# Performance work log

Hardware: AMD Instinct MI355X
Metric: run time of the kernel (lower is better)

The kernel has to match this reference:

```python
import jax, jax.numpy as jnp
import numpy as np

DELTA_VAR = 0.5
DELTA_DIST = 1.5
ALPHA, BETA, GAMMA = 1.0, 1.0, 0.001
EPS = 1e-8


def setup_inputs() -> dict:
    key = jax.random.key(0)
    k1, k2 = jax.random.split(key)
    N, D, C = 4_000_000, 16, 64
    features = jax.random.normal(k1, (N, D), dtype=jnp.float32)
    labels = jax.random.randint(k2, (N,), 0, C)  # every cluster id present w.h.p.
    return {"features": features, "labels": labels, "num_clusters": C}


def _discriminative_loss(features, labels, C):
    # per-cluster counts and means (scatter-mean, replaces the boolean-mask loop)
    ones = jnp.ones(features.shape[0], dtype=features.dtype)
    counts = jax.ops.segment_sum(ones, labels, num_segments=C)            # (C,)
    sums = jax.ops.segment_sum(features, labels, num_segments=C)          # (C, D)
    safe_counts = jnp.maximum(counts, 1.0)
    means = sums / safe_counts[:, None]                                   # (C, D)

    # intra-cluster (variance) loss: mean over clusters of mean hinge^2
    dists = jnp.linalg.norm(features - means[labels] + EPS, axis=1)       # (N,)
    hinge2 = jnp.square(jnp.maximum(dists - DELTA_VAR, 0.0))
    per_cluster = jax.ops.segment_sum(hinge2, labels, num_segments=C) / safe_counts
    var_loss = jnp.mean(per_cluster)

    # inter-cluster (distance) loss over all ordered pairs i != j
    diff = means[:, None, :] - means[None, :, :] + EPS                    # (C, C, D)
    pdist = jnp.linalg.norm(diff, axis=-1)                                # (C, C)
    h = jnp.square(jnp.maximum(2.0 * DELTA_DIST - pdist, 0.0))
    h = h * (1.0 - jnp.eye(C, dtype=h.dtype))
    dist_loss = jnp.sum(h) / float(C * (C - 1))

    # regularization: mean centroid norm
    reg_loss = jnp.mean(jnp.linalg.norm(means + EPS, axis=1))

    total = ALPHA * var_loss + BETA * dist_loss + GAMMA * reg_loss
    return jnp.stack([total, var_loss, dist_loss, reg_loss])  # (4,)


def reference(features, labels, num_clusters):
    return _discriminative_loss(features, labels, num_clusters)
```

## Files before the change

kernel.cpp:

```cpp
#include <hip/hip_runtime.h>
#include <math.h>

#define C 64
#define D 16
#define EPSF 1e-8f
#define DVAR 0.5f
#define DDIST 1.5f
#define FPSCALE 65536.0f
#define INV_FPSCALE (1.0f / 65536.0f)
#define VARSCALE 4294967296.0
#define INV_VARSCALE (1.0 / 4294967296.0)

__global__ __launch_bounds__(256) void k_zero(int* ws, int n) {
    int i = blockIdx.x * 256 + threadIdx.x;
    if (i < n) ws[i] = 0;
}

__global__ __launch_bounds__(256) void k_sums(const float4* __restrict__ f4,
                                              const int* __restrict__ labels, int N,
                                              int* __restrict__ g_sums,
                                              unsigned* __restrict__ g_cnt) {
    __shared__ int s_sums[C * 17];
    __shared__ unsigned s_cnt[C];
    int t = threadIdx.x;
    for (int i = t; i < C * 17; i += 256) s_sums[i] = 0;
    if (t < C) s_cnt[t] = 0u;
    __syncthreads();

    int ntiles = (N + 255) >> 8;
    for (int it = blockIdx.x; it < ntiles; it += gridDim.x) {
        int tile = ntiles - 1 - it;
        int p = (tile << 8) + t;
        if (p >= N) continue;
        int c = labels[p] & (C - 1);
        float4 a  = f4[4 * p + 0];
        float4 b  = f4[4 * p + 1];
        float4 cc = f4[4 * p + 2];
        float4 dd = f4[4 * p + 3];
        int* row = &s_sums[c * 17];
        atomicAdd(row + 0,  __float2int_rn(a.x  * FPSCALE));
        atomicAdd(row + 1,  __float2int_rn(a.y  * FPSCALE));
        atomicAdd(row + 2,  __float2int_rn(a.z  * FPSCALE));
        atomicAdd(row + 3,  __float2int_rn(a.w  * FPSCALE));
        atomicAdd(row + 4,  __float2int_rn(b.x  * FPSCALE));
        atomicAdd(row + 5,  __float2int_rn(b.y  * FPSCALE));
        atomicAdd(row + 6,  __float2int_rn(b.z  * FPSCALE));
        atomicAdd(row + 7,  __float2int_rn(b.w  * FPSCALE));
        atomicAdd(row + 8,  __float2int_rn(cc.x * FPSCALE));
        atomicAdd(row + 9,  __float2int_rn(cc.y * FPSCALE));
        atomicAdd(row + 10, __float2int_rn(cc.z * FPSCALE));
        atomicAdd(row + 11, __float2int_rn(cc.w * FPSCALE));
        atomicAdd(row + 12, __float2int_rn(dd.x * FPSCALE));
        atomicAdd(row + 13, __float2int_rn(dd.y * FPSCALE));
        atomicAdd(row + 14, __float2int_rn(dd.z * FPSCALE));
        atomicAdd(row + 15, __float2int_rn(dd.w * FPSCALE));
        atomicAdd(&s_cnt[c], 1u);
    }
    __syncthreads();
    for (int i = t; i < C * D; i += 256) {
        int c = i >> 4, d = i & 15;
        atomicAdd(&g_sums[i], s_sums[c * 17 + d]);
    }
    if (t < C) atomicAdd(&g_cnt[t], s_cnt[t]);
}

__global__ __launch_bounds__(256) void k_hinge(const float4* __restrict__ f4,
                                               const int* __restrict__ labels, int N,
                                               const int* __restrict__ g_sums,
                                               const unsigned* __restrict__ g_cnt,
                                               unsigned long long* __restrict__ g_var) {
    __shared__ float s_means[C * 20];
    __shared__ float s_w[C];
    __shared__ float s_red[256];
    int t = threadIdx.x;
    for (int i = t; i < C * D; i += 256) {
        int c = i >> 4, d = i & 15;
        s_means[c * 20 + d] = (float)g_sums[i] * INV_FPSCALE / fmaxf((float)g_cnt[c], 1.0f);
    }
    if (t < C) s_w[t] = 1.0f / (fmaxf((float)g_cnt[t], 1.0f) * (float)C);
    __syncthreads();

    float acc = 0.0f;
    int gid = blockIdx.x * 256 + t;
    int stride = gridDim.x * 256;
    for (int p = gid; p < N; p += stride) {
        int c = labels[p] & (C - 1);
        const float* m = &s_means[c * 20];
        float4 m0 = *(const float4*)(m + 0);
        float4 m1 = *(const float4*)(m + 4);
        float4 m2 = *(const float4*)(m + 8);
        float4 m3 = *(const float4*)(m + 12);
        float4 a  = f4[4 * p + 0];
        float4 b  = f4[4 * p + 1];
        float4 cc = f4[4 * p + 2];
        float4 dd = f4[4 * p + 3];
        float ss = 0.0f, dx;
        dx = a.x - m0.x + EPSF; ss += dx * dx;
        dx = a.y - m0.y + EPSF; ss += dx * dx;
        dx = a.z - m0.z + EPSF; ss += dx * dx;
        dx = a.w - m0.w + EPSF; ss += dx * dx;
        dx = b.x - m1.x + EPSF; ss += dx * dx;
        dx = b.y - m1.y + EPSF; ss += dx * dx;
        dx = b.z - m1.z + EPSF; ss += dx * dx;
        dx = b.w - m1.w + EPSF; ss += dx * dx;
        dx = cc.x - m2.x + EPSF; ss += dx * dx;
        dx = cc.y - m2.y + EPSF; ss += dx * dx;
        dx = cc.z - m2.z + EPSF; ss += dx * dx;
        dx = cc.w - m2.w + EPSF; ss += dx * dx;
        dx = dd.x - m3.x + EPSF; ss += dx * dx;
        dx = dd.y - m3.y + EPSF; ss += dx * dx;
        dx = dd.z - m3.z + EPSF; ss += dx * dx;
        dx = dd.w - m3.w + EPSF; ss += dx * dx;
        float h = fmaxf(sqrtf(ss) - DVAR, 0.0f);
        acc += h * h * s_w[c];
    }
    s_red[t] = acc;
    __syncthreads();
    for (int s = 128; s > 0; s >>= 1) {
        if (t < s) s_red[t] += s_red[t + s];
        __syncthreads();
    }
    if (t == 0) {
        unsigned long long q = (unsigned long long)((double)s_red[0] * VARSCALE + 0.5);
        atomicAdd(g_var, q);
    }
}

__global__ __launch_bounds__(256) void k_final(const int* __restrict__ g_sums,
                                               const unsigned* __restrict__ g_cnt,
                                               const unsigned long long* __restrict__ g_var,
                                               float* __restrict__ out) {
    __shared__ float s_m[C * 17];
    __shared__ float red[256];
    int t = threadIdx.x;
    for (int i = t; i < C * D; i += 256) {
        int c = i >> 4, d = i & 15;
        s_m[c * 17 + d] = (float)g_sums[i] * INV_FPSCALE / fmaxf((float)g_cnt[c], 1.0f);
    }
    __syncthreads();

    float var_loss = (float)((double)g_var[0] * INV_VARSCALE);

    float ds = 0.0f;
    for (int p = t; p < C * C; p += 256) {
        int i = p >> 6, j = p & 63;
        if (i != j) {
            float ss = 0.0f;
            #pragma unroll
            for (int d = 0; d < D; d++) {
                float df = s_m[i * 17 + d] - s_m[j * 17 + d] + EPSF;
                ss += df * df;
            }
            float h = fmaxf(2.0f * DDIST - sqrtf(ss), 0.0f);
            ds += h * h;
        }
    }
    red[t] = ds;
    __syncthreads();
    for (int s = 128; s > 0; s >>= 1) {
        if (t < s) red[t] += red[t + s];
        __syncthreads();
    }
    float dist_loss = red[0] / (float)(C * (C - 1));
    __syncthreads();

    float rg = 0.0f;
    if (t < C) {
        float ss = 0.0f;
        #pragma unroll
        for (int d = 0; d < D; d++) {
            float m = s_m[t * 17 + d] + EPSF;
            ss += m * m;
        }
        rg = sqrtf(ss);
    }
    red[t] = rg;
    __syncthreads();
    for (int s = 128; s > 0; s >>= 1) {
        if (t < s) red[t] += red[t + s];
        __syncthreads();
    }
    float reg_loss = red[0] / (float)C;

    if (t == 0) {
        out[0] = var_loss + dist_loss + 0.001f * reg_loss;
        out[1] = var_loss;
        out[2] = dist_loss;
        out[3] = reg_loss;
    }
}

extern "C" void kernel_launch(void* const* d_in, const int* in_sizes, int n_in,
                              void* d_out, int out_size, void* d_ws, size_t ws_size,
                              hipStream_t stream) {
    const float* features = (const float*)d_in[0];
    const int* labels = (const int*)d_in[1];
    int N = in_sizes[0] / D;

    int* ws = (int*)d_ws;
    int* g_sums = ws;
    unsigned* g_cnt = (unsigned*)(ws + 1024);
    unsigned long long* g_var = (unsigned long long*)(ws + 1088);
    float* out = (float*)d_out;

    hipLaunchKernelGGL(k_zero, dim3(5), dim3(256), 0, stream, ws, 1090);
    hipLaunchKernelGGL(k_sums, dim3(2048), dim3(256), 0, stream,
                       (const float4*)features, labels, N, g_sums, g_cnt);
    hipLaunchKernelGGL(k_hinge, dim3(2048), dim3(256), 0, stream,
                       (const float4*)features, labels, N, g_sums, g_cnt, g_var);
    hipLaunchKernelGGL(k_final, dim3(1), dim3(256), 0, stream, g_sums, g_cnt, g_var, out);
}
```

Measured before the change: 410.8 us.

## Split each point across four lanes for coalesced float4 loads in sums and hinge

```diff
diff --git a/kernel.cpp b/kernel.cpp
--- a/kernel.cpp
+++ b/kernel.cpp
@@ -27,34 +27,21 @@
     if (t < C) s_cnt[t] = 0u;
     __syncthreads();
 
-    int ntiles = (N + 255) >> 8;
+    int q = t & 3;
+    int pr = t >> 2;
+    int ntiles = (N + 63) >> 6;
     for (int it = blockIdx.x; it < ntiles; it += gridDim.x) {
         int tile = ntiles - 1 - it;
-        int p = (tile << 8) + t;
+        int p = (tile << 6) + pr;
         if (p >= N) continue;
         int c = labels[p] & (C - 1);
-        float4 a  = f4[4 * p + 0];
-        float4 b  = f4[4 * p + 1];
-        float4 cc = f4[4 * p + 2];
-        float4 dd = f4[4 * p + 3];
-        int* row = &s_sums[c * 17];
-        atomicAdd(row + 0,  __float2int_rn(a.x  * FPSCALE));
-        atomicAdd(row + 1,  __float2int_rn(a.y  * FPSCALE));
-        atomicAdd(row + 2,  __float2int_rn(a.z  * FPSCALE));
-        atomicAdd(row + 3,  __float2int_rn(a.w  * FPSCALE));
-        atomicAdd(row + 4,  __float2int_rn(b.x  * FPSCALE));
-        atomicAdd(row + 5,  __float2int_rn(b.y  * FPSCALE));
-        atomicAdd(row + 6,  __float2int_rn(b.z  * FPSCALE));
-        atomicAdd(row + 7,  __float2int_rn(b.w  * FPSCALE));
-        atomicAdd(row + 8,  __float2int_rn(cc.x * FPSCALE));
-        atomicAdd(row + 9,  __float2int_rn(cc.y * FPSCALE));
-        atomicAdd(row + 10, __float2int_rn(cc.z * FPSCALE));
-        atomicAdd(row + 11, __float2int_rn(cc.w * FPSCALE));
-        atomicAdd(row + 12, __float2int_rn(dd.x * FPSCALE));
-        atomicAdd(row + 13, __float2int_rn(dd.y * FPSCALE));
-        atomicAdd(row + 14, __float2int_rn(dd.z * FPSCALE));
-        atomicAdd(row + 15, __float2int_rn(dd.w * FPSCALE));
-        atomicAdd(&s_cnt[c], 1u);
+        float4 v = f4[(tile << 8) + t];
+        int* row = &s_sums[c * 17 + (q << 2)];
+        atomicAdd(row + 0, __float2int_rn(v.x * FPSCALE));
+        atomicAdd(row + 1, __float2int_rn(v.y * FPSCALE));
+        atomicAdd(row + 2, __float2int_rn(v.z * FPSCALE));
+        atomicAdd(row + 3, __float2int_rn(v.w * FPSCALE));
+        if (q == 0) atomicAdd(&s_cnt[c], 1u);
     }
     __syncthreads();
     for (int i = t; i < C * D; i += 256) {
@@ -69,7 +56,7 @@
                                                const int* __restrict__ g_sums,
                                                const unsigned* __restrict__ g_cnt,
                                                unsigned long long* __restrict__ g_var) {
-    __shared__ float s_means[C * 20];
+    __shared__ __align__(16) float s_means[C * 20];
     __shared__ float s_w[C];
     __shared__ float s_red[256];
     int t = threadIdx.x;
@@ -77,40 +64,26 @@
         int c = i >> 4, d = i & 15;
         s_means[c * 20 + d] = (float)g_sums[i] * INV_FPSCALE / fmaxf((float)g_cnt[c], 1.0f);
     }
-    if (t < C) s_w[t] = 1.0f / (fmaxf((float)g_cnt[t], 1.0f) * (float)C);
+    if (t < C) s_w[t] = 0.25f / (fmaxf((float)g_cnt[t], 1.0f) * (float)C);
     __syncthreads();
 
+    int q = t & 3;
+    int pr = t >> 2;
     float acc = 0.0f;
-    int gid = blockIdx.x * 256 + t;
-    int stride = gridDim.x * 256;
-    for (int p = gid; p < N; p += stride) {
+    int ntiles = (N + 63) >> 6;
+    for (int tile = blockIdx.x; tile < ntiles; tile += gridDim.x) {
+        int p = (tile << 6) + pr;
+        if (p >= N) continue;
         int c = labels[p] & (C - 1);
-        const float* m = &s_means[c * 20];
-        float4 m0 = *(const float4*)(m + 0);
-        float4 m1 = *(const float4*)(m + 4);
-        float4 m2 = *(const float4*)(m + 8);
-        float4 m3 = *(const float4*)(m + 12);
-        float4 a  = f4[4 * p + 0];
-        float4 b  = f4[4 * p + 1];
-        float4 cc = f4[4 * p + 2];
-        float4 dd = f4[4 * p + 3];
-        float ss = 0.0f, dx;
-        dx = a.x - m0.x + EPSF; ss += dx * dx;
-        dx = a.y - m0.y + EPSF; ss += dx * dx;
-        dx = a.z - m0.z + EPSF; ss += dx * dx;
-        dx = a.w - m0.w + EPSF; ss += dx * dx;
-        dx = b.x - m1.x + EPSF; ss += dx * dx;
-        dx = b.y - m1.y + EPSF; ss += dx * dx;
-        dx = b.z - m1.z + EPSF; ss += dx * dx;
-        dx = b.w - m1.w + EPSF; ss += dx * dx;
-        dx = cc.x - m2.x + EPSF; ss += dx * dx;
-        dx = cc.y - m2.y + EPSF; ss += dx * dx;
-        dx = cc.z - m2.z + EPSF; ss += dx * dx;
-        dx = cc.w - m2.w + EPSF; ss += dx * dx;
-        dx = dd.x - m3.x + EPSF; ss += dx * dx;
-        dx = dd.y - m3.y + EPSF; ss += dx * dx;
-        dx = dd.z - m3.z + EPSF; ss += dx * dx;
-        dx = dd.w - m3.w + EPSF; ss += dx * dx;
+        float4 v = f4[(tile << 8) + t];
+        float4 m = *(const float4*)&s_means[c * 20 + (q << 2)];
+        float dx, ss;
+        dx = v.x - m.x + EPSF; ss  = dx * dx;
+        dx = v.y - m.y + EPSF; ss += dx * dx;
+        dx = v.z - m.z + EPSF; ss += dx * dx;
+        dx = v.w - m.w + EPSF; ss += dx * dx;
+        ss += __shfl_xor(ss, 1);
+        ss += __shfl_xor(ss, 2);
         float h = fmaxf(sqrtf(ss) - DVAR, 0.0f);
         acc += h * h * s_w[c];
     }
@@ -121,8 +94,8 @@
         __syncthreads();
     }
     if (t == 0) {
-        unsigned long long q = (unsigned long long)((double)s_red[0] * VARSCALE + 0.5);
-        atomicAdd(g_var, q);
+        unsigned long long qv = (unsigned long long)((double)s_red[0] * VARSCALE + 0.5);
+        atomicAdd(g_var, qv);
     }
 }
 
```

Result: slower. 435.3 us (+6.0%).

## Fuse four kernels into one cooperative kernel with grid-wide syncs

Applied to the files above, without the earlier changes.

```diff
diff --git a/kernel.cpp b/kernel.cpp
--- a/kernel.cpp
+++ b/kernel.cpp
@@ -1,5 +1,8 @@
 #include <hip/hip_runtime.h>
+#include <hip/hip_cooperative_groups.h>
 #include <math.h>
+
+namespace cg = cooperative_groups;
 
 #define C 64
 #define D 16
@@ -10,31 +13,42 @@
 #define INV_FPSCALE (1.0f / 65536.0f)
 #define VARSCALE 4294967296.0
 #define INV_VARSCALE (1.0 / 4294967296.0)
+#define GRID 1024
 
-__global__ __launch_bounds__(256) void k_zero(int* ws, int n) {
-    int i = blockIdx.x * 256 + threadIdx.x;
-    if (i < n) ws[i] = 0;
-}
+__global__ __launch_bounds__(256, 4) void k_fused(const float4* __restrict__ f4,
+                                                  const int* __restrict__ labels, int N,
+                                                  int* __restrict__ ws,
+                                                  float* __restrict__ out) {
+    cg::grid_group grid = cg::this_grid();
+    int* g_sums = ws;
+    unsigned* g_cnt = (unsigned*)(ws + 1024);
+    unsigned long long* g_var = (unsigned long long*)(ws + 1088);
 
-__global__ __launch_bounds__(256) void k_sums(const float4* __restrict__ f4,
-                                              const int* __restrict__ labels, int N,
-                                              int* __restrict__ g_sums,
-                                              unsigned* __restrict__ g_cnt) {
     __shared__ int s_sums[C * 17];
     __shared__ unsigned s_cnt[C];
+    __shared__ __align__(16) float s_means[C * 20];
+    __shared__ float s_w[C];
+    __shared__ float s_red[256];
+
     int t = threadIdx.x;
+    int b = blockIdx.x;
+    int gid = b * 256 + t;
+    int nthr = gridDim.x * 256;
+
+    if (gid < 1090) ws[gid] = 0;
     for (int i = t; i < C * 17; i += 256) s_sums[i] = 0;
     if (t < C) s_cnt[t] = 0u;
-    __syncthreads();
+    __threadfence();
+    grid.sync();
 
     int ntiles = (N + 255) >> 8;
-    for (int it = blockIdx.x; it < ntiles; it += gridDim.x) {
+    for (int it = b; it < ntiles; it += gridDim.x) {
         int tile = ntiles - 1 - it;
         int p = (tile << 8) + t;
         if (p >= N) continue;
         int c = labels[p] & (C - 1);
         float4 a  = f4[4 * p + 0];
-        float4 b  = f4[4 * p + 1];
+        float4 bb = f4[4 * p + 1];
         float4 cc = f4[4 * p + 2];
         float4 dd = f4[4 * p + 3];
         int* row = &s_sums[c * 17];
@@ -42,10 +56,10 @@
         atomicAdd(row + 1,  __float2int_rn(a.y  * FPSCALE));
         atomicAdd(row + 2,  __float2int_rn(a.z  * FPSCALE));
         atomicAdd(row + 3,  __float2int_rn(a.w  * FPSCALE));
-        atomicAdd(row + 4,  __float2int_rn(b.x  * FPSCALE));
-        atomicAdd(row + 5,  __float2int_rn(b.y  * FPSCALE));
-        atomicAdd(row + 6,  __float2int_rn(b.z  * FPSCALE));
-        atomicAdd(row + 7,  __float2int_rn(b.w  * FPSCALE));
+        atomicAdd(row + 4,  __float2int_rn(bb.x * FPSCALE));
+        atomicAdd(row + 5,  __float2int_rn(bb.y * FPSCALE));
+        atomicAdd(row + 6,  __float2int_rn(bb.z * FPSCALE));
+        atomicAdd(row + 7,  __float2int_rn(bb.w * FPSCALE));
         atomicAdd(row + 8,  __float2int_rn(cc.x * FPSCALE));
         atomicAdd(row + 9,  __float2int_rn(cc.y * FPSCALE));
         atomicAdd(row + 10, __float2int_rn(cc.z * FPSCALE));
@@ -62,17 +76,9 @@
         atomicAdd(&g_sums[i], s_sums[c * 17 + d]);
     }
     if (t < C) atomicAdd(&g_cnt[t], s_cnt[t]);
-}
+    __threadfence();
+    grid.sync();
 
-__global__ __launch_bounds__(256) void k_hinge(const float4* __restrict__ f4,
-                                               const int* __restrict__ labels, int N,
-                                               const int* __restrict__ g_sums,
-                                               const unsigned* __restrict__ g_cnt,
-                                               unsigned long long* __restrict__ g_var) {
-    __shared__ float s_means[C * 20];
-    __shared__ float s_w[C];
-    __shared__ float s_red[256];
-    int t = threadIdx.x;
     for (int i = t; i < C * D; i += 256) {
         int c = i >> 4, d = i & 15;
         s_means[c * 20 + d] = (float)g_sums[i] * INV_FPSCALE / fmaxf((float)g_cnt[c], 1.0f);
@@ -81,9 +87,7 @@
     __syncthreads();
 
     float acc = 0.0f;
-    int gid = blockIdx.x * 256 + t;
-    int stride = gridDim.x * 256;
-    for (int p = gid; p < N; p += stride) {
+    for (int p = gid; p < N; p += nthr) {
         int c = labels[p] & (C - 1);
         const float* m = &s_means[c * 20];
         float4 m0 = *(const float4*)(m + 0);
@@ -91,7 +95,7 @@
         float4 m2 = *(const float4*)(m + 8);
         float4 m3 = *(const float4*)(m + 12);
         float4 a  = f4[4 * p + 0];
-        float4 b  = f4[4 * p + 1];
+        float4 bb = f4[4 * p + 1];
         float4 cc = f4[4 * p + 2];
         float4 dd = f4[4 * p + 3];
         float ss = 0.0f, dx;
@@ -99,10 +103,10 @@
         dx = a.y - m0.y + EPSF; ss += dx * dx;
         dx = a.z - m0.z + EPSF; ss += dx * dx;
         dx = a.w - m0.w + EPSF; ss += dx * dx;
-        dx = b.x - m1.x + EPSF; ss += dx * dx;
-        dx = b.y - m1.y + EPSF; ss += dx * dx;
-        dx = b.z - m1.z + EPSF; ss += dx * dx;
-        dx = b.w - m1.w + EPSF; ss += dx * dx;
+        dx = bb.x - m1.x + EPSF; ss += dx * dx;
+        dx = bb.y - m1.y + EPSF; ss += dx * dx;
+        dx = bb.z - m1.z + EPSF; ss += dx * dx;
+        dx = bb.w - m1.w + EPSF; ss += dx * dx;
         dx = cc.x - m2.x + EPSF; ss += dx * dx;
         dx = cc.y - m2.y + EPSF; ss += dx * dx;
         dx = cc.z - m2.z + EPSF; ss += dx * dx;
@@ -121,23 +125,13 @@
         __syncthreads();
     }
     if (t == 0) {
-        unsigned long long q = (unsigned long long)((double)s_red[0] * VARSCALE + 0.5);
-        atomicAdd(g_var, q);
+        unsigned long long qv = (unsigned long long)((double)s_red[0] * VARSCALE + 0.5);
+        atomicAdd(g_var, qv);
     }
-}
+    __threadfence();
+    grid.sync();
 
-__global__ __launch_bounds__(256) void k_final(const int* __restrict__ g_sums,
-                                               const unsigned* __restrict__ g_cnt,
-                                               const unsigned long long* __restrict__ g_var,
-                                               float* __restrict__ out) {
-    __shared__ float s_m[C * 17];
-    __shared__ float red[256];
-    int t = threadIdx.x;
-    for (int i = t; i < C * D; i += 256) {
-        int c = i >> 4, d = i & 15;
-        s_m[c * 17 + d] = (float)g_sums[i] * INV_FPSCALE / fmaxf((float)g_cnt[c], 1.0f);
-    }
-    __syncthreads();
+    if (b != 0) return;
 
     float var_loss = (float)((double)g_var[0] * INV_VARSCALE);
 
@@ -148,20 +142,20 @@
             float ss = 0.0f;
             #pragma unroll
             for (int d = 0; d < D; d++) {
-                float df = s_m[i * 17 + d] - s_m[j * 17 + d] + EPSF;
+                float df = s_means[i * 20 + d] - s_means[j * 20 + d] + EPSF;
                 ss += df * df;
             }
             float h = fmaxf(2.0f * DDIST - sqrtf(ss), 0.0f);
             ds += h * h;
         }
     }
-    red[t] = ds;
+    s_red[t] = ds;
     __syncthreads();
     for (int s = 128; s > 0; s >>= 1) {
-        if (t < s) red[t] += red[t + s];
+        if (t < s) s_red[t] += s_red[t + s];
         __syncthreads();
     }
-    float dist_loss = red[0] / (float)(C * (C - 1));
+    float dist_loss = s_red[0] / (float)(C * (C - 1));
     __syncthreads();
 
     float rg = 0.0f;
@@ -169,18 +163,18 @@
         float ss = 0.0f;
         #pragma unroll
         for (int d = 0; d < D; d++) {
-            float m = s_m[t * 17 + d] + EPSF;
+            float m = s_means[t * 20 + d] + EPSF;
             ss += m * m;
         }
         rg = sqrtf(ss);
     }
-    red[t] = rg;
+    s_red[t] = rg;
     __syncthreads();
     for (int s = 128; s > 0; s >>= 1) {
-        if (t < s) red[t] += red[t + s];
+        if (t < s) s_red[t] += s_red[t + s];
         __syncthreads();
     }
-    float reg_loss = red[0] / (float)C;
+    float reg_loss = s_red[0] / (float)C;
 
     if (t == 0) {
         out[0] = var_loss + dist_loss + 0.001f * reg_loss;
@@ -193,20 +187,12 @@
 extern "C" void kernel_launch(void* const* d_in, const int* in_sizes, int n_in,
                               void* d_out, int out_size, void* d_ws, size_t ws_size,
                               hipStream_t stream) {
-    const float* features = (const float*)d_in[0];
+    const float4* f4 = (const float4*)d_in[0];
     const int* labels = (const int*)d_in[1];
     int N = in_sizes[0] / D;
-
     int* ws = (int*)d_ws;
-    int* g_sums = ws;
-    unsigned* g_cnt = (unsigned*)(ws + 1024);
-    unsigned long long* g_var = (unsigned long long*)(ws + 1088);
     float* out = (float*)d_out;
 
-    hipLaunchKernelGGL(k_zero, dim3(5), dim3(256), 0, stream, ws, 1090);
-    hipLaunchKernelGGL(k_sums, dim3(2048), dim3(256), 0, stream,
-                       (const float4*)features, labels, N, g_sums, g_cnt);
-    hipLaunchKernelGGL(k_hinge, dim3(2048), dim3(256), 0, stream,
-                       (const float4*)features, labels, N, g_sums, g_cnt, g_var);
-    hipLaunchKernelGGL(k_final, dim3(1), dim3(256), 0, stream, g_sums, g_cnt, g_var, out);
+    void* args[] = {(void*)&f4, (void*)&labels, (void*)&N, (void*)&ws, (void*)&out};
+    hipLaunchCooperativeKernel((const void*)k_fused, dim3(GRID), dim3(256), args, 0, stream);
 }
```

Measured after the change: 933.8 us. 127% more time.

## Replace global atomics with per-block partial buffers and a separate reduce kernel

Applied to the files above, without the earlier changes.

```diff
diff --git a/kernel.cpp b/kernel.cpp
--- a/kernel.cpp
+++ b/kernel.cpp
@@ -11,30 +11,31 @@
 #define VARSCALE 4294967296.0
 #define INV_VARSCALE (1.0 / 4294967296.0)
 
-__global__ __launch_bounds__(256) void k_zero(int* ws, int n) {
-    int i = blockIdx.x * 256 + threadIdx.x;
-    if (i < n) ws[i] = 0;
-}
+#define NB 2048
+#define SLICE 1088
+
+#define GF0 (NB * SLICE)
+#define V0 (GF0 + 1088)
 
 __global__ __launch_bounds__(256) void k_sums(const float4* __restrict__ f4,
                                               const int* __restrict__ labels, int N,
-                                              int* __restrict__ g_sums,
-                                              unsigned* __restrict__ g_cnt) {
+                                              int* __restrict__ arr) {
     __shared__ int s_sums[C * 17];
     __shared__ unsigned s_cnt[C];
     int t = threadIdx.x;
+    int b = blockIdx.x;
     for (int i = t; i < C * 17; i += 256) s_sums[i] = 0;
     if (t < C) s_cnt[t] = 0u;
     __syncthreads();
 
     int ntiles = (N + 255) >> 8;
-    for (int it = blockIdx.x; it < ntiles; it += gridDim.x) {
+    for (int it = b; it < ntiles; it += NB) {
         int tile = ntiles - 1 - it;
         int p = (tile << 8) + t;
         if (p >= N) continue;
         int c = labels[p] & (C - 1);
         float4 a  = f4[4 * p + 0];
-        float4 b  = f4[4 * p + 1];
+        float4 bb = f4[4 * p + 1];
         float4 cc = f4[4 * p + 2];
         float4 dd = f4[4 * p + 3];
         int* row = &s_sums[c * 17];
@@ -42,10 +43,10 @@
         atomicAdd(row + 1,  __float2int_rn(a.y  * FPSCALE));
         atomicAdd(row + 2,  __float2int_rn(a.z  * FPSCALE));
         atomicAdd(row + 3,  __float2int_rn(a.w  * FPSCALE));
-        atomicAdd(row + 4,  __float2int_rn(b.x  * FPSCALE));
-        atomicAdd(row + 5,  __float2int_rn(b.y  * FPSCALE));
-        atomicAdd(row + 6,  __float2int_rn(b.z  * FPSCALE));
-        atomicAdd(row + 7,  __float2int_rn(b.w  * FPSCALE));
+        atomicAdd(row + 4,  __float2int_rn(bb.x * FPSCALE));
+        atomicAdd(row + 5,  __float2int_rn(bb.y * FPSCALE));
+        atomicAdd(row + 6,  __float2int_rn(bb.z * FPSCALE));
+        atomicAdd(row + 7,  __float2int_rn(bb.w * FPSCALE));
         atomicAdd(row + 8,  __float2int_rn(cc.x * FPSCALE));
         atomicAdd(row + 9,  __float2int_rn(cc.y * FPSCALE));
         atomicAdd(row + 10, __float2int_rn(cc.z * FPSCALE));
@@ -57,32 +58,50 @@
         atomicAdd(&s_cnt[c], 1u);
     }
     __syncthreads();
+    for (int i = t; i < SLICE; i += 256) {
+        int v = (i < C * D) ? s_sums[(i >> 4) * 17 + (i & 15)] : (int)s_cnt[i - C * D];
+        arr[b * SLICE + i] = v;
+    }
+}
+
+__global__ __launch_bounds__(256) void k_reduce(const int* __restrict__ arr,
+                                                int* __restrict__ g_final) {
+    __shared__ int s[256];
+    int o = blockIdx.x;
+    int t = threadIdx.x;
+    int part = 0;
+    #pragma unroll
+    for (int j = 0; j < NB / 256; j++)
+        part += arr[(t + j * 256) * SLICE + o];
+    s[t] = part;
+    __syncthreads();
+    for (int st = 128; st > 0; st >>= 1) {
+        if (t < st) s[t] += s[t + st];
+        __syncthreads();
+    }
+    if (t == 0) g_final[o] = s[0];
+}
+
+__global__ __launch_bounds__(256) void k_hinge(const float4* __restrict__ f4,
+                                               const int* __restrict__ labels, int N,
+                                               const int* __restrict__ g_final,
+                                               unsigned long long* __restrict__ g_var) {
+    __shared__ __align__(16) float s_means[C * 20];
+    __shared__ float s_w[C];
+    __shared__ float s_red[256];
+    int t = threadIdx.x;
+    int b = blockIdx.x;
     for (int i = t; i < C * D; i += 256) {
         int c = i >> 4, d = i & 15;
-        atomicAdd(&g_sums[i], s_sums[c * 17 + d]);
-    }
-    if (t < C) atomicAdd(&g_cnt[t], s_cnt[t]);
-}
-
-__global__ __launch_bounds__(256) void k_hinge(const float4* __restrict__ f4,
-                                               const int* __restrict__ labels, int N,
-                                               const int* __restrict__ g_sums,
-                                               const unsigned* __restrict__ g_cnt,
-                                               unsigned long long* __restrict__ g_var) {
-    __shared__ float s_means[C * 20];
-    __shared__ float s_w[C];
-    __shared__ float s_red[256];
-    int t = threadIdx.x;
-    for (int i = t; i < C * D; i += 256) {
-        int c = i >> 4, d = i & 15;
-        s_means[c * 20 + d] = (float)g_sums[i] * INV_FPSCALE / fmaxf((float)g_cnt[c], 1.0f);
-    }
-    if (t < C) s_w[t] = 1.0f / (fmaxf((float)g_cnt[t], 1.0f) * (float)C);
+        float cnt = fmaxf((float)g_final[C * D + c], 1.0f);
+        s_means[c * 20 + d] = (float)g_final[i] * INV_FPSCALE / cnt;
+    }
+    if (t < C) s_w[t] = 1.0f / (fmaxf((float)g_final[C * D + t], 1.0f) * (float)C);
     __syncthreads();
 
     float acc = 0.0f;
-    int gid = blockIdx.x * 256 + t;
-    int stride = gridDim.x * 256;
+    int gid = b * 256 + t;
+    int stride = NB * 256;
     for (int p = gid; p < N; p += stride) {
         int c = labels[p] & (C - 1);
         const float* m = &s_means[c * 20];
@@ -91,7 +110,7 @@
         float4 m2 = *(const float4*)(m + 8);
         float4 m3 = *(const float4*)(m + 12);
         float4 a  = f4[4 * p + 0];
-        float4 b  = f4[4 * p + 1];
+        float4 bb = f4[4 * p + 1];
         float4 cc = f4[4 * p + 2];
         float4 dd = f4[4 * p + 3];
         float ss = 0.0f, dx;
@@ -99,10 +118,10 @@
         dx = a.y - m0.y + EPSF; ss += dx * dx;
         dx = a.z - m0.z + EPSF; ss += dx * dx;
         dx = a.w - m0.w + EPSF; ss += dx * dx;
-        dx = b.x - m1.x + EPSF; ss += dx * dx;
-        dx = b.y - m1.y + EPSF; ss += dx * dx;
-        dx = b.z - m1.z + EPSF; ss += dx * dx;
-        dx = b.w - m1.w + EPSF; ss += dx * dx;
+        dx = bb.x - m1.x + EPSF; ss += dx * dx;
+        dx = bb.y - m1.y + EPSF; ss += dx * dx;
+        dx = bb.z - m1.z + EPSF; ss += dx * dx;
+        dx = bb.w - m1.w + EPSF; ss += dx * dx;
         dx = cc.x - m2.x + EPSF; ss += dx * dx;
         dx = cc.y - m2.y + EPSF; ss += dx * dx;
         dx = cc.z - m2.z + EPSF; ss += dx * dx;
@@ -120,26 +139,33 @@
         if (t < s) s_red[t] += s_red[t + s];
         __syncthreads();
     }
-    if (t == 0) {
-        unsigned long long q = (unsigned long long)((double)s_red[0] * VARSCALE + 0.5);
-        atomicAdd(g_var, q);
-    }
-}
-
-__global__ __launch_bounds__(256) void k_final(const int* __restrict__ g_sums,
-                                               const unsigned* __restrict__ g_cnt,
+    if (t == 0)
+        g_var[b] = (unsigned long long)((double)s_red[0] * VARSCALE + 0.5);
+}
+
+__global__ __launch_bounds__(256) void k_final(const int* __restrict__ g_final,
                                                const unsigned long long* __restrict__ g_var,
                                                float* __restrict__ out) {
     __shared__ float s_m[C * 17];
     __shared__ float red[256];
+    __shared__ unsigned long long red64[256];
     int t = threadIdx.x;
     for (int i = t; i < C * D; i += 256) {
         int c = i >> 4, d = i & 15;
-        s_m[c * 17 + d] = (float)g_sums[i] * INV_FPSCALE / fmaxf((float)g_cnt[c], 1.0f);
-    }
-    __syncthreads();
-
-    float var_loss = (float)((double)g_var[0] * INV_VARSCALE);
+        float cnt = fmaxf((float)g_final[C * D + c], 1.0f);
+        s_m[c * 17 + d] = (float)g_final[i] * INV_FPSCALE / cnt;
+    }
+    unsigned long long vq = 0ull;
+    #pragma unroll
+    for (int j = 0; j < NB / 256; j++) vq += g_var[t + j * 256];
+    red64[t] = vq;
+    __syncthreads();
+    for (int s = 128; s > 0; s >>= 1) {
+        if (t < s) red64[t] += red64[t + s];
+        __syncthreads();
+    }
+    float var_loss = (float)((double)red64[0] * INV_VARSCALE);
+    __syncthreads();
 
     float ds = 0.0f;
     for (int p = t; p < C * C; p += 256) {
@@ -193,20 +219,18 @@
 extern "C" void kernel_launch(void* const* d_in, const int* in_sizes, int n_in,
                               void* d_out, int out_size, void* d_ws, size_t ws_size,
                               hipStream_t stream) {
-    const float* features = (const float*)d_in[0];
+    const float4* f4 = (const float4*)d_in[0];
     const int* labels = (const int*)d_in[1];
     int N = in_sizes[0] / D;
 
     int* ws = (int*)d_ws;
-    int* g_sums = ws;
-    unsigned* g_cnt = (unsigned*)(ws + 1024);
-    unsigned long long* g_var = (unsigned long long*)(ws + 1088);
+    int* arr = ws;
+    int* g_final = ws + GF0;
+    unsigned long long* g_var = (unsigned long long*)(ws + V0);
     float* out = (float*)d_out;
 
-    hipLaunchKernelGGL(k_zero, dim3(5), dim3(256), 0, stream, ws, 1090);
-    hipLaunchKernelGGL(k_sums, dim3(2048), dim3(256), 0, stream,
-                       (const float4*)features, labels, N, g_sums, g_cnt);
-    hipLaunchKernelGGL(k_hinge, dim3(2048), dim3(256), 0, stream,
-                       (const float4*)features, labels, N, g_sums, g_cnt, g_var);
-    hipLaunchKernelGGL(k_final, dim3(1), dim3(256), 0, stream, g_sums, g_cnt, g_var, out);
-}
+    hipLaunchKernelGGL(k_sums, dim3(NB), dim3(256), 0, stream, f4, labels, N, arr);
+    hipLaunchKernelGGL(k_reduce, dim3(SLICE), dim3(256), 0, stream, arr, g_final);
+    hipLaunchKernelGGL(k_hinge, dim3(NB), dim3(256), 0, stream, f4, labels, N, g_final, g_var);
+    hipLaunchKernelGGL(k_final, dim3(1), dim3(256), 0, stream, g_final, g_var, out);
+}
```

Result: slower. 420.0 us (+2.2%).
